# Kernel optimization log

Measured on AMD Instinct MI355X. Metric: run time of the kernel, lower is better.

## Reference

```python
import jax, jax.numpy as jnp
import numpy as np

N_BITS = 8          # MULTIPLIER_N_BITS in MCT
SIGNED = True
THRESHOLD = 2.0
EPS = 1e-8
N_CLUSTERS = 16


def setup_inputs() -> dict:
    key = jax.random.key(0)
    kx, kc = jax.random.split(key)
    x = jax.random.normal(kx, (32, 128, 56, 56), dtype=jnp.float32)
    # integer-valued cluster centers inside the signed 8-bit range, as in MCT's LUT kmeans
    centers = jnp.sort(
        jax.random.randint(kc, (N_CLUSTERS,), -(2 ** (N_BITS - 1)), 2 ** (N_BITS - 1) - 1)
    ).astype(jnp.float32)
    return {"x": x, "cluster_centers": centers}


def reference(x, cluster_centers):
    signed = int(SIGNED)
    scale = 2.0 ** (N_BITS - signed)            # 128 for signed
    clip_max = 2 ** (N_BITS - 1) - 1 if SIGNED else 2 ** N_BITS - 1
    clip_min = -(2 ** (N_BITS - 1)) if SIGNED else 0
    # 1) scale into the 8-bit range and clip
    t = jnp.clip(x / (THRESHOLD + EPS) * scale, clip_min, clip_max)
    # 2) nearest cluster center (broadcast [..., 1] vs [K])
    assignments = jnp.argmin(jnp.abs(t[..., None] - cluster_centers), axis=-1)
    centers = cluster_centers[assignments]
    # 3) scale back to the original range
    return centers / scale * THRESHOLD
```

## Files before the change

kernel.cpp:

```cpp
#include <hip/hip_runtime.h>

#define NCLUST 16
#define TBL 512
#define EPT 8

__global__ __launch_bounds__(512) void build_table_kernel(
    const float* __restrict__ centers, float2* __restrict__ tbl)
{
    int b = threadIdx.x;
    float c[NCLUST];
#pragma unroll
    for (int k = 0; k < NCLUST; ++k) c[k] = centers[k];
    int cnt = 0;
#pragma unroll
    for (int k = 0; k < NCLUST; ++k)
        cnt += (fmaf(c[k], 2.0f, 256.0f) <= (float)b) ? 1 : 0;
    int j = cnt - 1;
    j = j < 0 ? 0 : (j > NCLUST - 2 ? NCLUST - 2 : j);
    tbl[b] = make_float2(c[j], c[j + 1]);
}

__device__ __forceinline__ float quant1(float xv, const float2* __restrict__ lut)
{
    float t = xv * 64.0f;
    t = fminf(fmaxf(t, -128.0f), 127.0f);
    float s = fmaf(t, 2.0f, 256.0f);
    int b = (int)s;
    float2 p = lut[b];
    float d0 = __builtin_fabsf(t - p.x);
    float d1 = __builtin_fabsf(t - p.y);
    return (d0 <= d1 ? p.x : p.y) * 0.015625f;
}

__global__ __launch_bounds__(256) void lut_fakequant_kernel(
    const float* __restrict__ x,
    const float2* __restrict__ tbl,
    float* __restrict__ out,
    int n4, int tail)
{
    __shared__ __align__(16) float2 lut[TBL];
    ((float4*)lut)[threadIdx.x] = ((const float4*)tbl)[threadIdx.x];
    __syncthreads();

    const float4* __restrict__ x4 = (const float4*)x;
    float4* __restrict__ o4 = (float4*)out;

    const int i0 = blockIdx.x * (256 * EPT / 4) + threadIdx.x;
    const int i1 = i0 + 256;
    const bool g0 = i0 < n4;
    const bool g1 = i1 < n4;

    float4 v0, v1;
    if (g0) v0 = x4[i0];
    if (g1) v1 = x4[i1];

    if (g0) {
        float4 r;
        r.x = quant1(v0.x, lut); r.y = quant1(v0.y, lut);
        r.z = quant1(v0.z, lut); r.w = quant1(v0.w, lut);
        o4[i0] = r;
    }
    if (g1) {
        float4 r;
        r.x = quant1(v1.x, lut); r.y = quant1(v1.y, lut);
        r.z = quant1(v1.z, lut); r.w = quant1(v1.w, lut);
        o4[i1] = r;
    }

    if (blockIdx.x == 0 && threadIdx.x < tail) {
        long long idx = (long long)n4 * 4 + threadIdx.x;
        out[idx] = quant1(x[idx], lut);
    }
}

extern "C" void kernel_launch(void* const* d_in, const int* in_sizes, int n_in,
                              void* d_out, int out_size, void* d_ws, size_t ws_size,
                              hipStream_t stream) {
    const float* x       = (const float*)d_in[0];
    const float* centers = (const float*)d_in[1];
    float* out           = (float*)d_out;
    float2* tbl          = (float2*)d_ws;

    const int n    = in_sizes[0];
    const int n4   = n / 4;
    const int tail = n - n4 * 4;

    build_table_kernel<<<1, TBL, 0, stream>>>(centers, tbl);

    const int f4_per_block = 256 * EPT / 4;
    const int grid = (n4 + f4_per_block - 1) / f4_per_block;
    lut_fakequant_kernel<<<grid, 256, 0, stream>>>(x, tbl, out, n4, tail);
}
```

Baseline: 102.2 us.

## Fuse LUT build into quantize kernel and process four float4s per thread

Drops the separate single-block table-build launch. Each block now rebuilds the 512-entry nearest-pair table in shared memory from the 16 centers, issuing its global loads first so the table build overlaps them. It also works in pre-scaled units, folding the 1/64 factor into the table, and doubles the elements per thread so there are fewer blocks. The cost is redundant per-block table construction, two syncs, and more registers per thread.

```diff
diff --git a/kernel.cpp b/kernel.cpp
--- a/kernel.cpp
+++ b/kernel.cpp
@@ -2,69 +2,70 @@
 
 #define NCLUST 16
 #define TBL 512
-#define EPT 8
-
-__global__ __launch_bounds__(512) void build_table_kernel(
-    const float* __restrict__ centers, float2* __restrict__ tbl)
-{
-    int b = threadIdx.x;
-    float c[NCLUST];
-#pragma unroll
-    for (int k = 0; k < NCLUST; ++k) c[k] = centers[k];
-    int cnt = 0;
-#pragma unroll
-    for (int k = 0; k < NCLUST; ++k)
-        cnt += (fmaf(c[k], 2.0f, 256.0f) <= (float)b) ? 1 : 0;
-    int j = cnt - 1;
-    j = j < 0 ? 0 : (j > NCLUST - 2 ? NCLUST - 2 : j);
-    tbl[b] = make_float2(c[j], c[j + 1]);
-}
+#define F4PT 4
 
 __device__ __forceinline__ float quant1(float xv, const float2* __restrict__ lut)
 {
-    float t = xv * 64.0f;
-    t = fminf(fmaxf(t, -128.0f), 127.0f);
-    float s = fmaf(t, 2.0f, 256.0f);
+    float u = fminf(fmaxf(xv, -2.0f), 1.984375f);
+    float s = fmaf(u, 128.0f, 256.0f);
     int b = (int)s;
     float2 p = lut[b];
-    float d0 = __builtin_fabsf(t - p.x);
-    float d1 = __builtin_fabsf(t - p.y);
-    return (d0 <= d1 ? p.x : p.y) * 0.015625f;
+    float d0 = __builtin_fabsf(u - p.x);
+    float d1 = __builtin_fabsf(u - p.y);
+    return d0 <= d1 ? p.x : p.y;
 }
 
 __global__ __launch_bounds__(256) void lut_fakequant_kernel(
     const float* __restrict__ x,
-    const float2* __restrict__ tbl,
+    const float* __restrict__ centers,
     float* __restrict__ out,
     int n4, int tail)
 {
     __shared__ __align__(16) float2 lut[TBL];
-    ((float4*)lut)[threadIdx.x] = ((const float4*)tbl)[threadIdx.x];
-    __syncthreads();
+    __shared__ float cent[NCLUST];
 
     const float4* __restrict__ x4 = (const float4*)x;
     float4* __restrict__ o4 = (float4*)out;
 
-    const int i0 = blockIdx.x * (256 * EPT / 4) + threadIdx.x;
-    const int i1 = i0 + 256;
-    const bool g0 = i0 < n4;
-    const bool g1 = i1 < n4;
+    const int base = blockIdx.x * (256 * F4PT) + threadIdx.x;
+    float4 v[F4PT];
+    bool gok[F4PT];
+#pragma unroll
+    for (int r = 0; r < F4PT; ++r) {
+        int idx = base + 256 * r;
+        gok[r] = idx < n4;
+        if (gok[r]) v[r] = x4[idx];
+    }
 
-    float4 v0, v1;
-    if (g0) v0 = x4[i0];
-    if (g1) v1 = x4[i1];
+    if (threadIdx.x < NCLUST) cent[threadIdx.x] = centers[threadIdx.x] * 0.015625f;
+    float g[NCLUST];
+#pragma unroll
+    for (int k = 0; k < NCLUST; ++k) g[k] = centers[k] * 0.015625f;
+    __syncthreads();
 
-    if (g0) {
-        float4 r;
-        r.x = quant1(v0.x, lut); r.y = quant1(v0.y, lut);
-        r.z = quant1(v0.z, lut); r.w = quant1(v0.w, lut);
-        o4[i0] = r;
+#pragma unroll
+    for (int r = 0; r < TBL / 256; ++r) {
+        int b = threadIdx.x + 256 * r;
+        float tb = (float)(b - 256) * 0.0078125f;
+        int cnt = 0;
+#pragma unroll
+        for (int k = 0; k < NCLUST; ++k) cnt += (g[k] <= tb) ? 1 : 0;
+        int j = cnt - 1;
+        j = j < 0 ? 0 : (j > NCLUST - 2 ? NCLUST - 2 : j);
+        lut[b] = make_float2(cent[j], cent[j + 1]);
     }
-    if (g1) {
-        float4 r;
-        r.x = quant1(v1.x, lut); r.y = quant1(v1.y, lut);
-        r.z = quant1(v1.z, lut); r.w = quant1(v1.w, lut);
-        o4[i1] = r;
+    __syncthreads();
+
+#pragma unroll
+    for (int r = 0; r < F4PT; ++r) {
+        if (gok[r]) {
+            float4 res;
+            res.x = quant1(v[r].x, lut);
+            res.y = quant1(v[r].y, lut);
+            res.z = quant1(v[r].z, lut);
+            res.w = quant1(v[r].w, lut);
+            o4[base + 256 * r] = res;
+        }
     }
 
     if (blockIdx.x == 0 && threadIdx.x < tail) {
@@ -79,15 +80,12 @@
     const float* x       = (const float*)d_in[0];
     const float* centers = (const float*)d_in[1];
     float* out           = (float*)d_out;
-    float2* tbl          = (float2*)d_ws;
 
     const int n    = in_sizes[0];
     const int n4   = n / 4;
     const int tail = n - n4 * 4;
 
-    build_table_kernel<<<1, TBL, 0, stream>>>(centers, tbl);
-
-    const int f4_per_block = 256 * EPT / 4;
+    const int f4_per_block = 256 * F4PT;
     const int grid = (n4 + f4_per_block - 1) / f4_per_block;
-    lut_fakequant_kernel<<<grid, 256, 0, stream>>>(x, tbl, out, n4, tail);
+    lut_fakequant_kernel<<<grid, 256, 0, stream>>>(x, centers, out, n4, tail);
 }
```

New measurement: 100.2 us. -2.0%, faster.
